# Optimization experiments

Hardware: AMD Instinct MI355X
Metric: run time of the kernel (lower is better)

The kernel has to match this reference:

```python
import jax, jax.numpy as jnp
import numpy as np

N_NODES = 50000
N_EDGES = 800000
N_GRAPHS = 512
IN_DIM = 256
HID = 512
N_CLASSES = 10
BN_EPS = 1e-5


def setup_inputs() -> dict:
    key = jax.random.key(0)
    ks = jax.random.split(key, 32)
    x = jax.random.normal(ks[0], (N_NODES, IN_DIM), dtype=jnp.float32)
    edge_index = jax.random.randint(ks[1], (2, N_EDGES), 0, N_NODES, dtype=jnp.int64)
    batch = jnp.sort(jax.random.randint(ks[2], (N_NODES,), 0, N_GRAPHS, dtype=jnp.int64))

    def lin(k, fan_in, fan_out):
        kw, kb = jax.random.split(k)
        s = 1.0 / np.sqrt(fan_in)
        w = jax.random.uniform(kw, (fan_in, fan_out), jnp.float32, -s, s)
        b = jax.random.uniform(kb, (fan_out,), jnp.float32, -s, s)
        return w, b

    inp = {"x": x, "edge_index": edge_index, "batch": batch}
    # GIN layer 0 MLP (in->hid->hid), layers 1,2 (hid->hid->hid)
    inp["w0a"], inp["b0a"] = lin(ks[3], IN_DIM, HID)
    inp["w0b"], inp["b0b"] = lin(ks[4], HID, HID)
    inp["w1a"], inp["b1a"] = lin(ks[5], HID, HID)
    inp["w1b"], inp["b1b"] = lin(ks[6], HID, HID)
    inp["w2a"], inp["b2a"] = lin(ks[7], HID, HID)
    inp["w2b"], inp["b2b"] = lin(ks[8], HID, HID)
    # BatchNorm affine params
    for i in range(3):
        inp[f"bn{i}_g"] = jnp.ones((HID,), jnp.float32)
        inp[f"bn{i}_b"] = jnp.zeros((HID,), jnp.float32)
    # classifier
    inp["clf_w1"], inp["clf_b1"] = lin(ks[9], HID, HID)
    inp["clf_w2"], inp["clf_b2"] = lin(ks[10], HID, N_CLASSES)
    return inp


def _gin_layer(h, src, dst, wa, ba, wb, bb, g, b):
    # sum-aggregate neighbors (source -> target), eps = 0 (PyG default)
    agg = jax.ops.segment_sum(h[src], dst, num_segments=N_NODES)
    z = h + agg
    # 2-layer MLP: Linear -> ReLU -> Linear
    z = jax.nn.relu(z @ wa + ba) @ wb + bb
    # BatchNorm1d with batch statistics (training mode, biased var) + affine
    mu = jnp.mean(z, axis=0)
    var = jnp.var(z, axis=0)
    z = (z - mu) * jax.lax.rsqrt(var + BN_EPS) * g + b
    return jax.nn.relu(z)


def reference(x, edge_index, batch,
              w0a, b0a, w0b, b0b,
              w1a, b1a, w1b, b1b,
              w2a, b2a, w2b, b2b,
              bn0_g, bn0_b, bn1_g, bn1_b, bn2_g, bn2_b,
              clf_w1, clf_b1, clf_w2, clf_b2):
    src, dst = edge_index[0], edge_index[1]
    h = _gin_layer(x, src, dst, w0a, b0a, w0b, b0b, bn0_g, bn0_b)
    h = _gin_layer(h, src, dst, w1a, b1a, w1b, b1b, bn1_g, bn1_b)
    h = _gin_layer(h, src, dst, w2a, b2a, w2b, b2b, bn2_g, bn2_b)
    # global add pool over graphs
    gpool = jax.ops.segment_sum(h, batch, num_segments=N_GRAPHS)  # [G, HID]
    # classifier (dropout = identity in eval)
    logits = jax.nn.relu(gpool @ clf_w1 + clf_b1) @ clf_w2 + clf_b2
    probs = jax.nn.softmax(logits, axis=1)
    preds = jnp.argmax(probs, axis=1)
    one_hot = jax.nn.one_hot(preds, N_CLASSES, dtype=logits.dtype)
    return (logits, probs, preds.astype(jnp.float32), one_hot)
```

## Files before the change

### kernel.cpp

```cpp
#include <hip/hip_runtime.h>

#define N_NODES 50000
#define N_EDGES 800000
#define N_GRAPHS 512
#define IN_DIM 256
#define HID 512
#define BN_EPS 1e-5f

typedef __attribute__((ext_vector_type(8))) short bf16x8;
typedef __attribute__((ext_vector_type(4))) float f32x4;

__device__ inline void split_bf16(float a, unsigned short& hi, unsigned short& lo) {
  unsigned u = __float_as_uint(a);
  hi = (unsigned short)(u >> 16);
  float fh = __uint_as_float(u & 0xFFFF0000u);
  float r = a - fh;
  lo = (unsigned short)(__float_as_uint(r) >> 16);
}

__device__ inline void split4_store(float4 v, unsigned short* hip, unsigned short* lop) {
  unsigned short h0, h1, h2, h3, l0, l1, l2, l3;
  split_bf16(v.x, h0, l0);
  split_bf16(v.y, h1, l1);
  split_bf16(v.z, h2, l2);
  split_bf16(v.w, h3, l3);
  uint2 hv, lv;
  hv.x = (unsigned)h0 | ((unsigned)h1 << 16);
  hv.y = (unsigned)h2 | ((unsigned)h3 << 16);
  lv.x = (unsigned)l0 | ((unsigned)l1 << 16);
  lv.y = (unsigned)l2 | ((unsigned)l3 << 16);
  *(uint2*)hip = hv;
  *(uint2*)lop = lv;
}

__device__ inline float4 bnrelu4(float4 v, float4 s, float4 h) {
  float4 o;
  o.x = fmaxf(fmaf(v.x, s.x, h.x), 0.f);
  o.y = fmaxf(fmaf(v.y, s.y, h.y), 0.f);
  o.z = fmaxf(fmaf(v.z, s.z, h.z), 0.f);
  o.w = fmaxf(fmaf(v.w, s.w, h.w), 0.f);
  return o;
}

__global__ __launch_bounds__(256) void hist_dst(const int* __restrict__ dst,
                                                int* __restrict__ deg) {
  for (int e = blockIdx.x * 256 + threadIdx.x; e < N_EDGES; e += gridDim.x * 256)
    atomicAdd(&deg[dst[e]], 1);
}

__global__ __launch_bounds__(1024) void scan_deg(const int* __restrict__ deg,
                                                 int* __restrict__ off,
                                                 int* __restrict__ cursor) {
  __shared__ int partial[1024];
  const int t = threadIdx.x;
  const int CHUNK = 49;
  const int base = t * CHUNK;
  int mysum = 0;
  for (int i = 0; i < CHUNK; ++i) {
    int idx = base + i;
    if (idx < N_NODES) mysum += deg[idx];
  }
  partial[t] = mysum;
  __syncthreads();
  for (int st = 1; st < 1024; st <<= 1) {
    int v = (t >= st) ? partial[t - st] : 0;
    __syncthreads();
    partial[t] += v;
    __syncthreads();
  }
  int run = partial[t] - mysum;
  for (int i = 0; i < CHUNK; ++i) {
    int idx = base + i;
    if (idx < N_NODES) {
      off[idx] = run;
      cursor[idx] = run;
      run += deg[idx];
    }
  }
  if (t == 1023) off[N_NODES] = N_EDGES;
}

__global__ __launch_bounds__(256) void fill_csr(const int* __restrict__ src,
                                                const int* __restrict__ dst,
                                                int* __restrict__ cursor,
                                                int* __restrict__ eidx) {
  for (int e = blockIdx.x * 256 + threadIdx.x; e < N_EDGES; e += gridDim.x * 256) {
    int p = atomicAdd(&cursor[dst[e]], 1);
    eidx[p] = src[e];
  }
}

template <int ROWF4, int HASBN>
__global__ __launch_bounds__(256) void agg_pk(const float4* __restrict__ h4,
                                              const int* __restrict__ off,
                                              const int* __restrict__ eidx,
                                              const float4* __restrict__ scale4,
                                              const float4* __restrict__ shift4,
                                              unsigned short* __restrict__ zp) {
  const int n = blockIdx.x * 4 + (threadIdx.x >> 6);
  if (n >= N_NODES) return;
  const int lane = threadIdx.x & 63;
  const int ROW = ROWF4 * 64;
  float4 sc[ROWF4], sh[ROWF4];
  if (HASBN) {
#pragma unroll
    for (int j = 0; j < ROWF4; ++j) {
      sc[j] = scale4[j * 64 + lane];
      sh[j] = shift4[j * 64 + lane];
    }
  }
  float4 v[ROWF4];
  const float4* hn = h4 + (long long)n * ROW;
#pragma unroll
  for (int j = 0; j < ROWF4; ++j) {
    float4 a = hn[j * 64 + lane];
    v[j] = HASBN ? bnrelu4(a, sc[j], sh[j]) : a;
  }

  int p = off[n];
  const int pe = off[n + 1];
  for (; p < pe; p += 8) {
    const float4* hp[8];
    float m[8];
#pragma unroll
    for (int e = 0; e < 8; ++e) {
      bool ok = (p + e) < pe;
      int idx = ok ? (p + e) : (pe - 1);
      hp[e] = h4 + (long long)eidx[idx] * ROW;
      m[e] = ok ? 1.f : 0.f;
    }
#pragma unroll
    for (int j = 0; j < ROWF4; ++j) {
      float4 t[8];
#pragma unroll
      for (int e = 0; e < 8; ++e) {
        t[e] = hp[e][j * 64 + lane];
        if (HASBN) t[e] = bnrelu4(t[e], sc[j], sh[j]);
      }
#pragma unroll
      for (int e = 0; e < 8; ++e) {
        v[j].x = fmaf(t[e].x, m[e], v[j].x);
        v[j].y = fmaf(t[e].y, m[e], v[j].y);
        v[j].z = fmaf(t[e].z, m[e], v[j].z);
        v[j].w = fmaf(t[e].w, m[e], v[j].w);
      }
    }
  }
  const int nd = n & 63, tile = n >> 6;
#pragma unroll
  for (int j = 0; j < ROWF4; ++j) {
    int cj = j * 64 + lane;
    int ks = cj >> 3, k4 = cj & 7;
    size_t base = ((size_t)tile * (ROWF4 * 8) + ks) * 4096 + (size_t)nd * 32 +
                  (size_t)k4 * 4;
    split4_store(v[j], zp + base, zp + base + 2048);
  }
}

template <int HASBN>
__global__ __launch_bounds__(256) void agg_pk_half(const float4* __restrict__ h4,
                                                   const int* __restrict__ off,
                                                   const int* __restrict__ eidx,
                                                   const float4* __restrict__ scale4,
                                                   const float4* __restrict__ shift4,
                                                   unsigned short* __restrict__ zp,
                                                   int jsel) {
  const int n = blockIdx.x * 4 + (threadIdx.x >> 6);
  if (n >= N_NODES) return;
  const int lane = threadIdx.x & 63;
  const int ROW = 128;
  const int cj = jsel * 64 + lane;
  float4 sc, sh;
  if (HASBN) {
    sc = scale4[cj];
    sh = shift4[cj];
  }
  const float4* hn = h4 + (long long)n * ROW;
  float4 a0 = hn[cj];
  float4 v = HASBN ? bnrelu4(a0, sc, sh) : a0;

  int p = off[n];
  const int pe = off[n + 1];
  for (; p < pe; p += 8) {
    const float4* hp[8];
    float m[8];
#pragma unroll
    for (int e = 0; e < 8; ++e) {
      bool ok = (p + e) < pe;
      int idx = ok ? (p + e) : (pe - 1);
      hp[e] = h4 + (long long)eidx[idx] * ROW;
      m[e] = ok ? 1.f : 0.f;
    }
    float4 t[8];
#pragma unroll
    for (int e = 0; e < 8; ++e) {
      t[e] = hp[e][cj];
      if (HASBN) t[e] = bnrelu4(t[e], sc, sh);
    }
#pragma unroll
    for (int e = 0; e < 8; ++e) {
      v.x = fmaf(t[e].x, m[e], v.x);
      v.y = fmaf(t[e].y, m[e], v.y);
      v.z = fmaf(t[e].z, m[e], v.z);
      v.w = fmaf(t[e].w, m[e], v.w);
    }
  }
  const int nd = n & 63, tile = n >> 6;
  const int ks = cj >> 3, k4 = cj & 7;
  size_t base = ((size_t)tile * 16 + ks) * 4096 + (size_t)nd * 32 + (size_t)k4 * 4;
  split4_store(v, zp + base, zp + base + 2048);
}

__global__ __launch_bounds__(256) void wt_build(const float* __restrict__ W,
                                                unsigned short* __restrict__ Wp,
                                                int KS) {
  int gid = blockIdx.x * 256 + threadIdx.x;
  int total = 2 * KS * 8192;
  if (gid >= total) return;
  int blk = gid >> 13;
  int rem = gid & 8191;
  int cf = rem >> 9;
  int q = (rem >> 7) & 3;
  int c = (rem >> 3) & 15;
  int j = rem & 7;
  int bx = blk / KS, ks = blk - bx * KS;
  int chan = bx * 256 + cf * 16 + c;
  int k = ks * 32 + q * 8 + j;
  float v = W[(size_t)k * 512 + chan];
  unsigned short h, l;
  split_bf16(v, h, l);
  Wp[(size_t)blk * 16384 + rem] = h;
  Wp[(size_t)blk * 16384 + 8192 + rem] = l;
}

template <int KS, int STATS, int PACKOUT>
__global__ __launch_bounds__(256, 2) void gemm_pk(const unsigned short* __restrict__ Ap,
                                                  const unsigned short* __restrict__ Wp,
                                                  const float* __restrict__ bias,
                                                  float* __restrict__ Cf,
                                                  unsigned short* __restrict__ Cp,
                                                  float* __restrict__ stat_sum,
                                                  float* __restrict__ stat_sq,
                                                  int N, int NTtiles, int relu) {
  const int wg = blockIdx.x;
  const int bx = (wg >> 3) & 1;
  const int tile = (wg >> 4) * 8 + (wg & 7);
  if (tile >= NTtiles) return;
  const int tid = threadIdx.x;
  const int wv = tid >> 6, ln = tid & 63;
  const int n0 = tile * 64;
  const int q = ln >> 4, ccs = ln & 15;

  f32x4 acc[4][4];
#pragma unroll
  for (int i = 0; i < 4; ++i)
#pragma unroll
    for (int j = 0; j < 4; ++j) acc[i][j] = f32x4{0.f, 0.f, 0.f, 0.f};

  const unsigned short* wp =
      Wp + ((size_t)bx * KS) * 16384 + (size_t)(wv * 4) * 512 + (size_t)ln * 8;
  const unsigned short* ap =
      Ap + (size_t)tile * KS * 4096 + (size_t)ccs * 32 + (size_t)q * 8;

  bf16x8 wh[2][4], wl[2][4], ah[2][4], al[2][4];

#define LOADSTG(B, KSI)                                      \
  {                                                          \
    const unsigned short* w_ = wp + (size_t)(KSI) * 16384;   \
    const unsigned short* a_ = ap + (size_t)(KSI) * 4096;    \
    _Pragma("unroll") for (int i_ = 0; i_ < 4; ++i_) {       \
      wh[B][i_] = *(const bf16x8*)(w_ + i_ * 512);           \
      wl[B][i_] = *(const bf16x8*)(w_ + 8192 + i_ * 512);    \
      ah[B][i_] = *(const bf16x8*)(a_ + i_ * 512);           \
      al[B][i_] = *(const bf16x8*)(a_ + 2048 + i_ * 512);    \
    }                                                        \
  }

  LOADSTG(0, 0)
#pragma unroll
  for (int ks = 0; ks < KS; ++ks) {
    const int cur = ks & 1;
    if (ks + 1 < KS) LOADSTG(cur ^ 1, ks + 1)
#pragma unroll
    for (int i = 0; i < 4; ++i)
#pragma unroll
      for (int j = 0; j < 4; ++j) {
        acc[i][j] = __builtin_amdgcn_mfma_f32_16x16x32_bf16(wh[cur][i], ah[cur][j], acc[i][j], 0, 0, 0);
        acc[i][j] = __builtin_amdgcn_mfma_f32_16x16x32_bf16(wh[cur][i], al[cur][j], acc[i][j], 0, 0, 0);
        acc[i][j] = __builtin_amdgcn_mfma_f32_16x16x32_bf16(wl[cur][i], ah[cur][j], acc[i][j], 0, 0, 0);
      }
  }
#undef LOADSTG

  const int chanb = bx * 256 + wv * 64 + (ln >> 4) * 4;
  float4 s4[4], q4[4];
  if (STATS) {
#pragma unroll
    for (int i = 0; i < 4; ++i) {
      s4[i] = make_float4(0.f, 0.f, 0.f, 0.f);
      q4[i] = make_float4(0.f, 0.f, 0.f, 0.f);
    }
  }
#pragma unroll
  for (int j = 0; j < 4; ++j) {
    int node = n0 + j * 16 + (ln & 15);
    bool valid = node < N;
    int nd = node & 63;
    int tile2 = node >> 6;
#pragma unroll
    for (int i = 0; i < 4; ++i) {
      int chan = chanb + i * 16;
      float4 bv = *(const float4*)(bias + chan);
      f32x4 a = acc[i][j];
      float4 o;
      o.x = a[0] + bv.x;
      o.y = a[1] + bv.y;
      o.z = a[2] + bv.z;
      o.w = a[3] + bv.w;
      if (relu) {
        o.x = fmaxf(o.x, 0.f);
        o.y = fmaxf(o.y, 0.f);
        o.z = fmaxf(o.z, 0.f);
        o.w = fmaxf(o.w, 0.f);
      }
      if (PACKOUT) {
        if (valid) {
          size_t base = ((size_t)tile2 * 16 + (size_t)(chan >> 5)) * 4096 +
                        (size_t)nd * 32 + (size_t)(chan & 31);
          split4_store(o, Cp + base, Cp + base + 2048);
        }
      } else {
        if (valid) *(float4*)(Cf + (size_t)node * 512 + chan) = o;
        if (STATS) {
          if (!valid) o = make_float4(0.f, 0.f, 0.f, 0.f);
          s4[i].x += o.x; s4[i].y += o.y; s4[i].z += o.z; s4[i].w += o.w;
          q4[i].x += o.x * o.x; q4[i].y += o.y * o.y;
          q4[i].z += o.z * o.z; q4[i].w += o.w * o.w;
        }
      }
    }
  }
  if (STATS) {
#pragma unroll
    for (int i = 0; i < 4; ++i) {
#pragma unroll
      for (int mask = 1; mask < 16; mask <<= 1) {
        s4[i].x += __shfl_xor(s4[i].x, mask);
        s4[i].y += __shfl_xor(s4[i].y, mask);
        s4[i].z += __shfl_xor(s4[i].z, mask);
        s4[i].w += __shfl_xor(s4[i].w, mask);
        q4[i].x += __shfl_xor(q4[i].x, mask);
        q4[i].y += __shfl_xor(q4[i].y, mask);
        q4[i].z += __shfl_xor(q4[i].z, mask);
        q4[i].w += __shfl_xor(q4[i].w, mask);
      }
    }
    if ((ln & 15) == 0) {
#pragma unroll
      for (int i = 0; i < 4; ++i) {
        int chan = chanb + i * 16;
        atomicAdd(&stat_sum[chan + 0], s4[i].x);
        atomicAdd(&stat_sum[chan + 1], s4[i].y);
        atomicAdd(&stat_sum[chan + 2], s4[i].z);
        atomicAdd(&stat_sum[chan + 3], s4[i].w);
        atomicAdd(&stat_sq[chan + 0], q4[i].x);
        atomicAdd(&stat_sq[chan + 1], q4[i].y);
        atomicAdd(&stat_sq[chan + 2], q4[i].z);
        atomicAdd(&stat_sq[chan + 3], q4[i].w);
      }
    }
  }
}

__global__ __launch_bounds__(512) void bn_finalize(const float* __restrict__ sum,
                                                   const float* __restrict__ sumsq,
                                                   const float* __restrict__ g,
                                                   const float* __restrict__ b,
                                                   float* __restrict__ scale,
                                                   float* __restrict__ shift) {
  const int c = threadIdx.x;
  const float invN = 1.0f / (float)N_NODES;
  float mu = sum[c] * invN;
  float var = sumsq[c] * invN - mu * mu;
  float sc = rsqrtf(var + BN_EPS) * g[c];
  scale[c] = sc;
  shift[c] = fmaf(-mu, sc, b[c]);
}

__global__ __launch_bounds__(512) void pool_bounds(const int* __restrict__ batch,
                                                   int* __restrict__ gstart) {
  const int g = threadIdx.x;
  int lo = 0, hi = N_NODES;
  while (lo < hi) {
    int mid = (lo + hi) >> 1;
    if (batch[mid] < g) lo = mid + 1;
    else hi = mid;
  }
  gstart[g] = lo;
  if (g == 0) gstart[N_GRAPHS] = N_NODES;
}

__global__ __launch_bounds__(128) void gpool_bn(const float4* __restrict__ z4,
                                                const int* __restrict__ gstart,
                                                const float4* __restrict__ scale4,
                                                const float4* __restrict__ shift4,
                                                unsigned short* __restrict__ gpp) {
  const int g = blockIdx.x;
  const int t = threadIdx.x;
  const int s = gstart[g], e = gstart[g + 1];
  const float4 sc = scale4[t], sh = shift4[t];
  float4 acc = make_float4(0.f, 0.f, 0.f, 0.f);
  for (int n = s; n < e; ++n) {
    float4 v = bnrelu4(z4[(size_t)n * 128 + t], sc, sh);
    acc.x += v.x;
    acc.y += v.y;
    acc.z += v.z;
    acc.w += v.w;
  }
  const int tile = g >> 6, nd = g & 63;
  const int ks = t >> 3, k4 = t & 7;
  size_t base = ((size_t)tile * 16 + ks) * 4096 + (size_t)nd * 32 + (size_t)k4 * 4;
  split4_store(acc, gpp + base, gpp + base + 2048);
}

__global__ __launch_bounds__(64) void clf2_softmax(const float* __restrict__ hidden,
                                                   const float* __restrict__ w2,
                                                   const float* __restrict__ b2,
                                                   float* __restrict__ out) {
  const int g = blockIdx.x;
  const int lane = threadIdx.x;
  float acc[10];
#pragma unroll
  for (int j = 0; j < 10; ++j) acc[j] = 0.f;
  for (int k = lane; k < HID; k += 64) {
    float hv = hidden[(long long)g * HID + k];
#pragma unroll
    for (int j = 0; j < 10; ++j) acc[j] += hv * w2[k * 10 + j];
  }
#pragma unroll
  for (int j = 0; j < 10; ++j) {
    for (int o = 32; o > 0; o >>= 1) acc[j] += __shfl_down(acc[j], o);
  }
  if (lane == 0) {
    float lg[10], pb[10];
    float mx = -1e30f;
#pragma unroll
    for (int j = 0; j < 10; ++j) {
      lg[j] = acc[j] + b2[j];
      mx = fmaxf(mx, lg[j]);
    }
    float se = 0.f;
#pragma unroll
    for (int j = 0; j < 10; ++j) {
      pb[j] = __expf(lg[j] - mx);
      se += pb[j];
    }
    float inv = 1.f / se;
    int am = 0;
    float best = lg[0];
#pragma unroll
    for (int j = 1; j < 10; ++j) {
      if (lg[j] > best) { best = lg[j]; am = j; }
    }
#pragma unroll
    for (int j = 0; j < 10; ++j) out[g * 10 + j] = lg[j];
#pragma unroll
    for (int j = 0; j < 10; ++j) out[N_GRAPHS * 10 + g * 10 + j] = pb[j] * inv;
    out[2 * N_GRAPHS * 10 + g] = (float)am;
#pragma unroll
    for (int j = 0; j < 10; ++j)
      out[2 * N_GRAPHS * 10 + N_GRAPHS + g * 10 + j] = (j == am) ? 1.f : 0.f;
  }
}

extern "C" void kernel_launch(void* const* d_in, const int* in_sizes, int n_in,
                              void* d_out, int out_size, void* d_ws, size_t ws_size,
                              hipStream_t stream) {
  const float* x = (const float*)d_in[0];
  const int* src = (const int*)d_in[1];
  const int* dstE = src + N_EDGES;
  const int* batch = (const int*)d_in[2];
  const float* w0a = (const float*)d_in[3];
  const float* b0a = (const float*)d_in[4];
  const float* w0b = (const float*)d_in[5];
  const float* b0b = (const float*)d_in[6];
  const float* w1a = (const float*)d_in[7];
  const float* b1a = (const float*)d_in[8];
  const float* w1b = (const float*)d_in[9];
  const float* b1b = (const float*)d_in[10];
  const float* w2a = (const float*)d_in[11];
  const float* b2a = (const float*)d_in[12];
  const float* w2b = (const float*)d_in[13];
  const float* b2b = (const float*)d_in[14];
  const float* bng[3] = {(const float*)d_in[15], (const float*)d_in[17], (const float*)d_in[19]};
  const float* bnb[3] = {(const float*)d_in[16], (const float*)d_in[18], (const float*)d_in[20]};
  const float* clf_w1 = (const float*)d_in[21];
  const float* clf_b1 = (const float*)d_in[22];
  const float* clf_w2 = (const float*)d_in[23];
  const float* clf_b2 = (const float*)d_in[24];
  float* out = (float*)d_out;

  const long long BUF = 25624576LL;
  float* bufA = (float*)d_ws;
  float* bufB = bufA + BUF;
  float* bnsum = bufB + BUF;
  float* bnsq = bnsum + 512;
  float* scale = bnsq + 512;
  float* shift = scale + 512;
  unsigned short* gpPack = (unsigned short*)(shift + 512);
  float* hidden = (float*)(gpPack + 524288);
  unsigned short* wp0a = (unsigned short*)(hidden + 262144);
  unsigned short* wp0b = wp0a + 262144;
  unsigned short* wp1a = wp0b + 524288;
  unsigned short* wp1b = wp1a + 524288;
  unsigned short* wp2a = wp1b + 524288;
  unsigned short* wp2b = wp2a + 524288;
  unsigned short* wpc1 = wp2b + 524288;
  int* deg = (int*)(wpc1 + 524288);
  int* off = deg + N_NODES;
  int* cursor = off + N_NODES + 1;
  int* eidx = cursor + N_NODES;
  int* gstart = eidx + N_EDGES;

  hipMemsetAsync(deg, 0, N_NODES * sizeof(int), stream);
  hipLaunchKernelGGL(hist_dst, dim3(3125), dim3(256), 0, stream, dstE, deg);
  hipLaunchKernelGGL(scan_deg, dim3(1), dim3(1024), 0, stream, deg, off, cursor);
  hipLaunchKernelGGL(fill_csr, dim3(3125), dim3(256), 0, stream, src, dstE, cursor, eidx);
  hipLaunchKernelGGL(pool_bounds, dim3(1), dim3(512), 0, stream, batch, gstart);

  hipLaunchKernelGGL(wt_build, dim3(512), dim3(256), 0, stream, w0a, wp0a, 8);
  hipLaunchKernelGGL(wt_build, dim3(1024), dim3(256), 0, stream, w0b, wp0b, 16);
  hipLaunchKernelGGL(wt_build, dim3(1024), dim3(256), 0, stream, w1a, wp1a, 16);
  hipLaunchKernelGGL(wt_build, dim3(1024), dim3(256), 0, stream, w1b, wp1b, 16);
  hipLaunchKernelGGL(wt_build, dim3(1024), dim3(256), 0, stream, w2a, wp2a, 16);
  hipLaunchKernelGGL(wt_build, dim3(1024), dim3(256), 0, stream, w2b, wp2b, 16);
  hipLaunchKernelGGL(wt_build, dim3(1024), dim3(256), 0, stream, clf_w1, wpc1, 16);

  const unsigned short* wpa[3] = {wp0a, wp1a, wp2a};
  const unsigned short* wpb[3] = {wp0b, wp1b, wp2b};
  const float* ba[3] = {b0a, b1a, b2a};
  const float* bb[3] = {b0b, b1b, b2b};

  const int NT = (N_NODES + 63) / 64;
  const int GB = ((NT + 7) / 8) * 16;
  const int nagg = (N_NODES + 3) / 4;

  float* P = bufA;
  float* Q = bufB;
  for (int layer = 0; layer < 3; ++layer) {
    if (layer == 0) {
      hipLaunchKernelGGL((agg_pk<1, 0>), dim3(nagg), dim3(256), 0, stream,
                         (const float4*)x, off, eidx, nullptr, nullptr,
                         (unsigned short*)Q);
    } else {
      hipLaunchKernelGGL((agg_pk_half<1>), dim3(nagg), dim3(256), 0, stream,
                         (const float4*)P, off, eidx, (const float4*)scale,
                         (const float4*)shift, (unsigned short*)Q, 0);
      hipLaunchKernelGGL((agg_pk_half<1>), dim3(nagg), dim3(256), 0, stream,
                         (const float4*)P, off, eidx, (const float4*)scale,
                         (const float4*)shift, (unsigned short*)Q, 1);
    }
    { float* t = P; P = Q; Q = t; }
    if (layer == 0) {
      hipLaunchKernelGGL((gemm_pk<8, 0, 1>), dim3(GB), dim3(256), 0, stream,
                         (const unsigned short*)P, wpa[layer], ba[layer],
                         (float*)nullptr, (unsigned short*)Q, nullptr, nullptr,
                         N_NODES, NT, 1);
    } else {
      hipLaunchKernelGGL((gemm_pk<16, 0, 1>), dim3(GB), dim3(256), 0, stream,
                         (const unsigned short*)P, wpa[layer], ba[layer],
                         (float*)nullptr, (unsigned short*)Q, nullptr, nullptr,
                         N_NODES, NT, 1);
    }
    { float* t = P; P = Q; Q = t; }
    hipMemsetAsync(bnsum, 0, 2 * 512 * sizeof(float), stream);
    hipLaunchKernelGGL((gemm_pk<16, 1, 0>), dim3(GB), dim3(256), 0, stream,
                       (const unsigned short*)P, wpb[layer], bb[layer],
                       Q, (unsigned short*)nullptr, bnsum, bnsq,
                       N_NODES, NT, 0);
    { float* t = P; P = Q; Q = t; }
    hipLaunchKernelGGL(bn_finalize, dim3(1), dim3(512), 0, stream,
                       bnsum, bnsq, bng[layer], bnb[layer], scale, shift);
  }

  hipLaunchKernelGGL(gpool_bn, dim3(N_GRAPHS), dim3(128), 0, stream,
                     (const float4*)P, gstart, (const float4*)scale,
                     (const float4*)shift, gpPack);
  hipLaunchKernelGGL((gemm_pk<16, 0, 0>), dim3(16), dim3(256), 0, stream,
                     (const unsigned short*)gpPack, wpc1, clf_b1,
                     hidden, (unsigned short*)nullptr, nullptr, nullptr,
                     N_GRAPHS, 8, 1);
  hipLaunchKernelGGL(clf2_softmax, dim3(N_GRAPHS), dim3(64), 0, stream,
                     hidden, clf_w2, clf_b2, out);
}
```

Measured before the change: 1.629 ms.

## Stage GEMM operand tiles through LDS with direct global-to-LDS loads

Replaces the register double-buffered direct global loads in the packed bf16x3 GEMM with per-K-step staging of the W and A tiles into shared memory via global_load_lds, followed by LDS reads into MFMA operands. The A tile is now fetched once per workgroup and shared across waves instead of each wave loading it separately, which cuts redundant global traffic. In exchange the loop is single-buffered with two barriers per step, so loads are no longer overlapped with MFMA work, and the occupancy hint in launch_bounds is dropped.

```diff
diff --git a/kernel.cpp b/kernel.cpp
--- a/kernel.cpp
+++ b/kernel.cpp
@@ -9,6 +9,13 @@
 
 typedef __attribute__((ext_vector_type(8))) short bf16x8;
 typedef __attribute__((ext_vector_type(4))) float f32x4;
+
+#define AS1 __attribute__((address_space(1)))
+#define AS3 __attribute__((address_space(3)))
+
+__device__ inline void gload_lds16(const unsigned short* g, unsigned short* l) {
+  __builtin_amdgcn_global_load_lds((const AS1 void*)g, (AS3 void*)l, 16, 0, 0);
+}
 
 __device__ inline void split_bf16(float a, unsigned short& hi, unsigned short& lo) {
   unsigned u = __float_as_uint(a);
@@ -234,14 +241,15 @@
 }
 
 template <int KS, int STATS, int PACKOUT>
-__global__ __launch_bounds__(256, 2) void gemm_pk(const unsigned short* __restrict__ Ap,
-                                                  const unsigned short* __restrict__ Wp,
-                                                  const float* __restrict__ bias,
-                                                  float* __restrict__ Cf,
-                                                  unsigned short* __restrict__ Cp,
-                                                  float* __restrict__ stat_sum,
-                                                  float* __restrict__ stat_sq,
-                                                  int N, int NTtiles, int relu) {
+__global__ __launch_bounds__(256) void gemm_pk(const unsigned short* __restrict__ Ap,
+                                               const unsigned short* __restrict__ Wp,
+                                               const float* __restrict__ bias,
+                                               float* __restrict__ Cf,
+                                               unsigned short* __restrict__ Cp,
+                                               float* __restrict__ stat_sum,
+                                               float* __restrict__ stat_sq,
+                                               int N, int NTtiles, int relu) {
+  __shared__ unsigned short lds[20480];
   const int wg = blockIdx.x;
   const int bx = (wg >> 3) & 1;
   const int tile = (wg >> 4) * 8 + (wg & 7);
@@ -257,40 +265,41 @@
 #pragma unroll
     for (int j = 0; j < 4; ++j) acc[i][j] = f32x4{0.f, 0.f, 0.f, 0.f};
 
-  const unsigned short* wp =
-      Wp + ((size_t)bx * KS) * 16384 + (size_t)(wv * 4) * 512 + (size_t)ln * 8;
-  const unsigned short* ap =
-      Ap + (size_t)tile * KS * 4096 + (size_t)ccs * 32 + (size_t)q * 8;
-
-  bf16x8 wh[2][4], wl[2][4], ah[2][4], al[2][4];
-
-#define LOADSTG(B, KSI)                                      \
-  {                                                          \
-    const unsigned short* w_ = wp + (size_t)(KSI) * 16384;   \
-    const unsigned short* a_ = ap + (size_t)(KSI) * 4096;    \
-    _Pragma("unroll") for (int i_ = 0; i_ < 4; ++i_) {       \
-      wh[B][i_] = *(const bf16x8*)(w_ + i_ * 512);           \
-      wl[B][i_] = *(const bf16x8*)(w_ + 8192 + i_ * 512);    \
-      ah[B][i_] = *(const bf16x8*)(a_ + i_ * 512);           \
-      al[B][i_] = *(const bf16x8*)(a_ + 2048 + i_ * 512);    \
-    }                                                        \
-  }
-
-  LOADSTG(0, 0)
-#pragma unroll
+  const unsigned short* wblk0 = Wp + (size_t)bx * KS * 16384;
+  const unsigned short* ablk0 = Ap + (size_t)tile * KS * 4096;
+
   for (int ks = 0; ks < KS; ++ks) {
-    const int cur = ks & 1;
-    if (ks + 1 < KS) LOADSTG(cur ^ 1, ks + 1)
+    const unsigned short* wblk = wblk0 + (size_t)ks * 16384;
+    const unsigned short* ablk = ablk0 + (size_t)ks * 4096;
+#pragma unroll
+    for (int c = 0; c < 8; ++c)
+      gload_lds16(wblk + (wv * 8 + c) * 512 + ln * 8, &lds[(wv * 8 + c) * 512]);
+#pragma unroll
+    for (int c = 0; c < 2; ++c)
+      gload_lds16(ablk + (wv * 2 + c) * 512 + ln * 8, &lds[16384 + (wv * 2 + c) * 512]);
+    __syncthreads();
+
+    bf16x8 wh[4], wl[4], ah[4], al[4];
+#pragma unroll
+    for (int i = 0; i < 4; ++i) {
+      wh[i] = *(const bf16x8*)&lds[(wv * 4 + i) * 512 + ln * 8];
+      wl[i] = *(const bf16x8*)&lds[8192 + (wv * 4 + i) * 512 + ln * 8];
+    }
+#pragma unroll
+    for (int j = 0; j < 4; ++j) {
+      ah[j] = *(const bf16x8*)&lds[16384 + j * 512 + ccs * 32 + q * 8];
+      al[j] = *(const bf16x8*)&lds[18432 + j * 512 + ccs * 32 + q * 8];
+    }
 #pragma unroll
     for (int i = 0; i < 4; ++i)
 #pragma unroll
       for (int j = 0; j < 4; ++j) {
-        acc[i][j] = __builtin_amdgcn_mfma_f32_16x16x32_bf16(wh[cur][i], ah[cur][j], acc[i][j], 0, 0, 0);
-        acc[i][j] = __builtin_amdgcn_mfma_f32_16x16x32_bf16(wh[cur][i], al[cur][j], acc[i][j], 0, 0, 0);
-        acc[i][j] = __builtin_amdgcn_mfma_f32_16x16x32_bf16(wl[cur][i], ah[cur][j], acc[i][j], 0, 0, 0);
+        acc[i][j] = __builtin_amdgcn_mfma_f32_16x16x32_bf16(wh[i], ah[j], acc[i][j], 0, 0, 0);
+        acc[i][j] = __builtin_amdgcn_mfma_f32_16x16x32_bf16(wh[i], al[j], acc[i][j], 0, 0, 0);
+        acc[i][j] = __builtin_amdgcn_mfma_f32_16x16x32_bf16(wl[i], ah[j], acc[i][j], 0, 0, 0);
       }
-  }
-#undef LOADSTG
+    __syncthreads();
+  }
 
   const int chanb = bx * 256 + wv * 64 + (ln >> 4) * 4;
   float4 s4[4], q4[4];
```

Result: no change. 1.630 ms (+0.1%).

## Compute two node tiles per workgroup to reuse weight fragments in GEMM

Applied to the files above, without the earlier changes.

Each GEMM workgroup now processes two 64-node tiles, sharing each loaded weight fragment across both tiles' MFMAs, and the grid becomes 2D (column half by tile pair). The register double-buffering of the previous version is dropped in favour of loading the current stage only, and launch bounds drop to one workgroup per SIMD set to leave room for twice the accumulators. The goal is to halve weight loads per MFMA; the cost is lower occupancy and less load/compute overlap, with the swizzled tile ordering removed.

```diff
diff --git a/kernel.cpp b/kernel.cpp
--- a/kernel.cpp
+++ b/kernel.cpp
@@ -234,7 +234,7 @@
 }
 
 template <int KS, int STATS, int PACKOUT>
-__global__ __launch_bounds__(256, 2) void gemm_pk(const unsigned short* __restrict__ Ap,
+__global__ __launch_bounds__(256, 1) void gemm_pk(const unsigned short* __restrict__ Ap,
                                                   const unsigned short* __restrict__ Wp,
                                                   const float* __restrict__ bias,
                                                   float* __restrict__ Cf,
@@ -242,55 +242,57 @@
                                                   float* __restrict__ stat_sum,
                                                   float* __restrict__ stat_sq,
                                                   int N, int NTtiles, int relu) {
-  const int wg = blockIdx.x;
-  const int bx = (wg >> 3) & 1;
-  const int tile = (wg >> 4) * 8 + (wg & 7);
-  if (tile >= NTtiles) return;
+  const int bx = blockIdx.x;
+  const int t0 = blockIdx.y * 2;
+  const int t1r = t0 + 1;
+  const bool has1 = t1r < NTtiles;
+  const int t1 = has1 ? t1r : t0;
   const int tid = threadIdx.x;
   const int wv = tid >> 6, ln = tid & 63;
-  const int n0 = tile * 64;
   const int q = ln >> 4, ccs = ln & 15;
 
-  f32x4 acc[4][4];
+  f32x4 acc0[4][4], acc1[4][4];
 #pragma unroll
   for (int i = 0; i < 4; ++i)
 #pragma unroll
-    for (int j = 0; j < 4; ++j) acc[i][j] = f32x4{0.f, 0.f, 0.f, 0.f};
+    for (int j = 0; j < 4; ++j) {
+      acc0[i][j] = f32x4{0.f, 0.f, 0.f, 0.f};
+      acc1[i][j] = f32x4{0.f, 0.f, 0.f, 0.f};
+    }
 
   const unsigned short* wp =
       Wp + ((size_t)bx * KS) * 16384 + (size_t)(wv * 4) * 512 + (size_t)ln * 8;
-  const unsigned short* ap =
-      Ap + (size_t)tile * KS * 4096 + (size_t)ccs * 32 + (size_t)q * 8;
-
-  bf16x8 wh[2][4], wl[2][4], ah[2][4], al[2][4];
-
-#define LOADSTG(B, KSI)                                      \
-  {                                                          \
-    const unsigned short* w_ = wp + (size_t)(KSI) * 16384;   \
-    const unsigned short* a_ = ap + (size_t)(KSI) * 4096;    \
-    _Pragma("unroll") for (int i_ = 0; i_ < 4; ++i_) {       \
-      wh[B][i_] = *(const bf16x8*)(w_ + i_ * 512);           \
-      wl[B][i_] = *(const bf16x8*)(w_ + 8192 + i_ * 512);    \
-      ah[B][i_] = *(const bf16x8*)(a_ + i_ * 512);           \
-      al[B][i_] = *(const bf16x8*)(a_ + 2048 + i_ * 512);    \
-    }                                                        \
-  }
-
-  LOADSTG(0, 0)
-#pragma unroll
+  const unsigned short* ap0 =
+      Ap + (size_t)t0 * KS * 4096 + (size_t)ccs * 32 + (size_t)q * 8;
+  const unsigned short* ap1 =
+      Ap + (size_t)t1 * KS * 4096 + (size_t)ccs * 32 + (size_t)q * 8;
+
   for (int ks = 0; ks < KS; ++ks) {
-    const int cur = ks & 1;
-    if (ks + 1 < KS) LOADSTG(cur ^ 1, ks + 1)
+    const unsigned short* w = wp + (size_t)ks * 16384;
+    const unsigned short* a0 = ap0 + (size_t)ks * 4096;
+    const unsigned short* a1 = ap1 + (size_t)ks * 4096;
+    bf16x8 wh[4], wl[4], a0h[4], a0l[4], a1h[4], a1l[4];
+#pragma unroll
+    for (int i = 0; i < 4; ++i) {
+      wh[i] = *(const bf16x8*)(w + i * 512);
+      wl[i] = *(const bf16x8*)(w + 8192 + i * 512);
+      a0h[i] = *(const bf16x8*)(a0 + i * 512);
+      a0l[i] = *(const bf16x8*)(a0 + 2048 + i * 512);
+      a1h[i] = *(const bf16x8*)(a1 + i * 512);
+      a1l[i] = *(const bf16x8*)(a1 + 2048 + i * 512);
+    }
 #pragma unroll
     for (int i = 0; i < 4; ++i)
 #pragma unroll
       for (int j = 0; j < 4; ++j) {
-        acc[i][j] = __builtin_amdgcn_mfma_f32_16x16x32_bf16(wh[cur][i], ah[cur][j], acc[i][j], 0, 0, 0);
-        acc[i][j] = __builtin_amdgcn_mfma_f32_16x16x32_bf16(wh[cur][i], al[cur][j], acc[i][j], 0, 0, 0);
-        acc[i][j] = __builtin_amdgcn_mfma_f32_16x16x32_bf16(wl[cur][i], ah[cur][j], acc[i][j], 0, 0, 0);
+        acc0[i][j] = __builtin_amdgcn_mfma_f32_16x16x32_bf16(wh[i], a0h[j], acc0[i][j], 0, 0, 0);
+        acc0[i][j] = __builtin_amdgcn_mfma_f32_16x16x32_bf16(wh[i], a0l[j], acc0[i][j], 0, 0, 0);
+        acc0[i][j] = __builtin_amdgcn_mfma_f32_16x16x32_bf16(wl[i], a0h[j], acc0[i][j], 0, 0, 0);
+        acc1[i][j] = __builtin_amdgcn_mfma_f32_16x16x32_bf16(wh[i], a1h[j], acc1[i][j], 0, 0, 0);
+        acc1[i][j] = __builtin_amdgcn_mfma_f32_16x16x32_bf16(wh[i], a1l[j], acc1[i][j], 0, 0, 0);
+        acc1[i][j] = __builtin_amdgcn_mfma_f32_16x16x32_bf16(wl[i], a1h[j], acc1[i][j], 0, 0, 0);
       }
   }
-#undef LOADSTG
 
   const int chanb = bx * 256 + wv * 64 + (ln >> 4) * 4;
   float4 s4[4], q4[4];
@@ -301,45 +303,53 @@
       q4[i] = make_float4(0.f, 0.f, 0.f, 0.f);
     }
   }
-#pragma unroll
-  for (int j = 0; j < 4; ++j) {
-    int node = n0 + j * 16 + (ln & 15);
-    bool valid = node < N;
-    int nd = node & 63;
-    int tile2 = node >> 6;
-#pragma unroll
-    for (int i = 0; i < 4; ++i) {
-      int chan = chanb + i * 16;
-      float4 bv = *(const float4*)(bias + chan);
-      f32x4 a = acc[i][j];
-      float4 o;
-      o.x = a[0] + bv.x;
-      o.y = a[1] + bv.y;
-      o.z = a[2] + bv.z;
-      o.w = a[3] + bv.w;
-      if (relu) {
-        o.x = fmaxf(o.x, 0.f);
-        o.y = fmaxf(o.y, 0.f);
-        o.z = fmaxf(o.z, 0.f);
-        o.w = fmaxf(o.w, 0.f);
-      }
-      if (PACKOUT) {
-        if (valid) {
-          size_t base = ((size_t)tile2 * 16 + (size_t)(chan >> 5)) * 4096 +
-                        (size_t)nd * 32 + (size_t)(chan & 31);
-          split4_store(o, Cp + base, Cp + base + 2048);
-        }
-      } else {
-        if (valid) *(float4*)(Cf + (size_t)node * 512 + chan) = o;
-        if (STATS) {
-          if (!valid) o = make_float4(0.f, 0.f, 0.f, 0.f);
-          s4[i].x += o.x; s4[i].y += o.y; s4[i].z += o.z; s4[i].w += o.w;
-          q4[i].x += o.x * o.x; q4[i].y += o.y * o.y;
-          q4[i].z += o.z * o.z; q4[i].w += o.w * o.w;
-        }
-      }
-    }
-  }
+
+#define EPILOGUE(ACC, TILE, ACTIVE)                                              \
+  {                                                                              \
+    const int n0_ = (TILE)*64;                                                   \
+    _Pragma("unroll") for (int j = 0; j < 4; ++j) {                              \
+      int node = n0_ + j * 16 + (ln & 15);                                       \
+      bool valid = (ACTIVE) && node < N;                                         \
+      int nd = node & 63;                                                        \
+      int tile2 = node >> 6;                                                     \
+      _Pragma("unroll") for (int i = 0; i < 4; ++i) {                            \
+        int chan = chanb + i * 16;                                               \
+        float4 bv = *(const float4*)(bias + chan);                               \
+        f32x4 a = ACC[i][j];                                                     \
+        float4 o;                                                                \
+        o.x = a[0] + bv.x;                                                       \
+        o.y = a[1] + bv.y;                                                       \
+        o.z = a[2] + bv.z;                                                       \
+        o.w = a[3] + bv.w;                                                       \
+        if (relu) {                                                              \
+          o.x = fmaxf(o.x, 0.f);                                                 \
+          o.y = fmaxf(o.y, 0.f);                                                 \
+          o.z = fmaxf(o.z, 0.f);                                                 \
+          o.w = fmaxf(o.w, 0.f);                                                 \
+        }                                                                        \
+        if (PACKOUT) {                                                           \
+          if (valid) {                                                           \
+            size_t base = ((size_t)tile2 * 16 + (size_t)(chan >> 5)) * 4096 +    \
+                          (size_t)nd * 32 + (size_t)(chan & 31);                 \
+            split4_store(o, Cp + base, Cp + base + 2048);                        \
+          }                                                                      \
+        } else {                                                                 \
+          if (valid) *(float4*)(Cf + (size_t)node * 512 + chan) = o;             \
+          if (STATS) {                                                           \
+            if (!valid) o = make_float4(0.f, 0.f, 0.f, 0.f);                     \
+            s4[i].x += o.x; s4[i].y += o.y; s4[i].z += o.z; s4[i].w += o.w;      \
+            q4[i].x += o.x * o.x; q4[i].y += o.y * o.y;                          \
+            q4[i].z += o.z * o.z; q4[i].w += o.w * o.w;                          \
+          }                                                                      \
+        }                                                                        \
+      }                                                                          \
+    }                                                                            \
+  }
+
+  EPILOGUE(acc0, t0, true)
+  EPILOGUE(acc1, t1r, has1)
+#undef EPILOGUE
+
   if (STATS) {
 #pragma unroll
     for (int i = 0; i < 4; ++i) {
@@ -542,7 +552,7 @@
   const float* bb[3] = {b0b, b1b, b2b};
 
   const int NT = (N_NODES + 63) / 64;
-  const int GB = ((NT + 7) / 8) * 16;
+  const int NTP = (NT + 1) / 2;
   const int nagg = (N_NODES + 3) / 4;
 
   float* P = bufA;
@@ -562,19 +572,19 @@
     }
     { float* t = P; P = Q; Q = t; }
     if (layer == 0) {
-      hipLaunchKernelGGL((gemm_pk<8, 0, 1>), dim3(GB), dim3(256), 0, stream,
+      hipLaunchKernelGGL((gemm_pk<8, 0, 1>), dim3(2, NTP), dim3(256), 0, stream,
                          (const unsigned short*)P, wpa[layer], ba[layer],
                          (float*)nullptr, (unsigned short*)Q, nullptr, nullptr,
                          N_NODES, NT, 1);
     } else {
-      hipLaunchKernelGGL((gemm_pk<16, 0, 1>), dim3(GB), dim3(256), 0, stream,
+      hipLaunchKernelGGL((gemm_pk<16, 0, 1>), dim3(2, NTP), dim3(256), 0, stream,
                          (const unsigned short*)P, wpa[layer], ba[layer],
                          (float*)nullptr, (unsigned short*)Q, nullptr, nullptr,
                          N_NODES, NT, 1);
     }
     { float* t = P; P = Q; Q = t; }
     hipMemsetAsync(bnsum, 0, 2 * 512 * sizeof(float), stream);
-    hipLaunchKernelGGL((gemm_pk<16, 1, 0>), dim3(GB), dim3(256), 0, stream,
+    hipLaunchKernelGGL((gemm_pk<16, 1, 0>), dim3(2, NTP), dim3(256), 0, stream,
                        (const unsigned short*)P, wpb[layer], bb[layer],
                        Q, (unsigned short*)nullptr, bnsum, bnsq,
                        N_NODES, NT, 0);
@@ -586,7 +596,7 @@
   hipLaunchKernelGGL(gpool_bn, dim3(N_GRAPHS), dim3(128), 0, stream,
                      (const float4*)P, gstart, (const float4*)scale,
                      (const float4*)shift, gpPack);
-  hipLaunchKernelGGL((gemm_pk<16, 0, 0>), dim3(16), dim3(256), 0, stream,
+  hipLaunchKernelGGL((gemm_pk<16, 0, 0>), dim3(2, 4), dim3(256), 0, stream,
                      (const unsigned short*)gpPack, wpc1, clf_b1,
                      hidden, (unsigned short*)nullptr, nullptr, nullptr,
                      N_GRAPHS, 8, 1);
```

Result: slower. 1.871 ms (+14.8%).
